# Kernel tuning notes

Hardware: AMD Instinct MI355X
Metric: run time of the kernel (lower is better)

Reference implementation:

```python
import jax, jax.numpy as jnp
import numpy as np

HEADS = 4
DIM_HEAD = 32


def setup_inputs() -> dict:
    key = jax.random.key(0)
    k1, k2, k3, k4 = jax.random.split(key, 4)
    b, dim, t = 8, 64, 16384
    inner = HEADS * DIM_HEAD  # 128
    x = jax.random.normal(k1, (b, dim, t), dtype=jnp.float32)
    # Conv1d(dim, inner*3, kernel=1, bias=False) -> weight (3*inner, dim)
    w_qkv = jax.random.normal(k2, (3 * inner, dim), dtype=jnp.float32) * (1.0 / np.sqrt(dim))
    # Conv1d(inner, dim, kernel=1) -> weight (dim, inner), bias (dim,)
    w_out = jax.random.normal(k3, (dim, inner), dtype=jnp.float32) * (1.0 / np.sqrt(inner))
    b_out = jax.random.normal(k4, (dim,), dtype=jnp.float32) * 0.01
    return {"x": x, "w_qkv": w_qkv, "w_out": w_out, "b_out": b_out}


def reference(x, w_qkv, w_out, b_out):
    b, c, t = x.shape
    h, dh = HEADS, DIM_HEAD
    # 1x1 conv == per-timestep matmul: (b, 3*inner, t)
    qkv = jnp.einsum('oc,bct->bot', w_qkv, x)
    q, k, v = jnp.split(qkv, 3, axis=1)
    q = q.reshape(b, h, dh, t)
    k = k.reshape(b, h, dh, t)
    v = v.reshape(b, h, dh, t)
    q = jax.nn.softmax(q, axis=-1)   # softmax over time
    k = jax.nn.softmax(k, axis=-2)   # softmax over head-dim d
    # einsum('bhdt,bhds->bhds', k, v): sums k over t, broadcast-scales v
    context = jnp.einsum('bhdt,bhds->bhds', k, v)
    # einsum('bhdt,bhds->bhdt', q, context): sums context over s, scales q
    out = jnp.einsum('bhdt,bhds->bhdt', q, context)
    out = out.reshape(b, h * dh, t)
    # to_out 1x1 conv with bias
    return jnp.einsum('oc,bct->bot', w_out, out) + b_out[None, :, None]
```

## Files before the change

kernel.cpp:

```cpp
#include <hip/hip_runtime.h>
#include <math.h>


typedef short short8 __attribute__((ext_vector_type(8)));
typedef short short4s __attribute__((ext_vector_type(4)));
typedef float f32x4 __attribute__((ext_vector_type(4)));

namespace {
constexpr int NB = 8;
constexpr int NC = 64;
constexpr int NT = 16384;
constexpr int NI = 128;
constexpr int TBK = 256;
constexpr int CPB = NT / TBK;
constexpr int NBLK = NB * CPB;
constexpr int XSP = 72;
constexpr int PTP = 136;
constexpr int PT  = 32;
constexpr int REP = 8;

constexpr int WS_ZQ   = 0;
constexpr int WS_KSUM = WS_ZQ + REP * NB * NI;
constexpr int WS_XSUM = WS_KSUM + REP * NB * NI;
constexpr int WS_NFLOAT = WS_XSUM + REP * NB * NC;
}

__device__ __forceinline__ unsigned short f2bf(float f) {
  unsigned u = __float_as_uint(f);
  u += 0x7fffu + ((u >> 16) & 1u);
  return (unsigned short)(u >> 16);
}

template <bool XS>
__device__ __forceinline__ void stage_x(const float* __restrict__ xb, int t0,
                                        unsigned short* xs, float* xsum_dst, int tid) {
  const int c = tid >> 2, tq = tid & 3;
  const float4* xr = (const float4*)(xb + (size_t)c * NT + t0);
  float s = 0.f;
#pragma unroll 4
  for (int i = 0; i < 16; ++i) {
    const int tv = tq + 4 * i;
    float4 v = xr[tv];
    if (XS) s += (v.x + v.y) + (v.z + v.w);
    const int t = 4 * tv;
    xs[(t + 0) * XSP + c] = f2bf(v.x);
    xs[(t + 1) * XSP + c] = f2bf(v.y);
    xs[(t + 2) * XSP + c] = f2bf(v.z);
    xs[(t + 3) * XSP + c] = f2bf(v.w);
  }
  if (XS) {
    s += __shfl_xor(s, 1, 64);
    s += __shfl_xor(s, 2, 64);
    if (tq == 0) atomicAdd(xsum_dst + c, s);
  }
}

__device__ __forceinline__ void load_aq(const float* __restrict__ wqkv, int w,
                                        int lm, int quad, short8 aq[2][2]) {
#pragma unroll
  for (int tile = 0; tile < 2; ++tile)
#pragma unroll
    for (int s = 0; s < 2; ++s) {
      const float* pq = wqkv + (size_t)(32 * w + tile * 16 + lm) * NC + s * 32 + quad * 8;
#pragma unroll
      for (int j = 0; j < 8; ++j) aq[tile][s][j] = (short)f2bf(pq[j]);
    }
}

__global__ __launch_bounds__(256) void la_stats(
    const float* __restrict__ x, const float* __restrict__ wqkv,
    float* __restrict__ ws)
{
  __shared__ __align__(16) unsigned short xs[TBK * XSP];

  const int bid = blockIdx.x;
  const int b = bid >> 6, chunk = bid & 63;
  const int rep = chunk & (REP - 1);
  const int tid = threadIdx.x, lane = tid & 63;
  const int w = __builtin_amdgcn_readfirstlane(tid >> 6);
  const int lm = lane & 15, quad = lane >> 4;
  const float* xb = x + (size_t)b * NC * NT;

  stage_x<true>(xb, chunk * TBK, xs, ws + WS_XSUM + (rep * NB + b) * NC, tid);

  short8 aq[2][2], ak[2][2];
  load_aq(wqkv, w, lm, quad, aq);
#pragma unroll
  for (int tile = 0; tile < 2; ++tile)
#pragma unroll
    for (int s = 0; s < 2; ++s) {
      const float* pk = wqkv + (size_t)(NI + 32 * w + tile * 16 + lm) * NC + s * 32 + quad * 8;
#pragma unroll
      for (int j = 0; j < 8; ++j) ak[tile][s][j] = (short)f2bf(pk[j]);
    }

  float zq_acc[2][4] = {};
  float ks_acc[2][4] = {};
  __syncthreads();

  for (int tc = 0; tc < TBK / 16; ++tc) {
    short8 bf[2];
#pragma unroll
    for (int s = 0; s < 2; ++s)
      bf[s] = *(const short8*)&xs[(tc * 16 + lm) * XSP + s * 32 + quad * 8];
    f32x4 cq[2] = {{0,0,0,0},{0,0,0,0}}, ck[2] = {{0,0,0,0},{0,0,0,0}};
#pragma unroll
    for (int tile = 0; tile < 2; ++tile)
#pragma unroll
      for (int s = 0; s < 2; ++s) {
        cq[tile] = __builtin_amdgcn_mfma_f32_16x16x32_bf16(aq[tile][s], bf[s], cq[tile], 0, 0, 0);
        ck[tile] = __builtin_amdgcn_mfma_f32_16x16x32_bf16(ak[tile][s], bf[s], ck[tile], 0, 0, 0);
      }
    float ke[2][4];
    float zt = 0.f;
#pragma unroll
    for (int tile = 0; tile < 2; ++tile)
#pragma unroll
      for (int r = 0; r < 4; ++r) {
        zq_acc[tile][r] += __expf(cq[tile][r]);
        float e = __expf(ck[tile][r]);
        ke[tile][r] = e;
        zt += e;
      }
    zt += __shfl_xor(zt, 16, 64);
    zt += __shfl_xor(zt, 32, 64);
    const float rz = __builtin_amdgcn_rcpf(zt);
#pragma unroll
    for (int tile = 0; tile < 2; ++tile)
#pragma unroll
      for (int r = 0; r < 4; ++r)
        ks_acc[tile][r] = fmaf(ke[tile][r], rz, ks_acc[tile][r]);
  }

#pragma unroll
  for (int tile = 0; tile < 2; ++tile)
#pragma unroll
    for (int r = 0; r < 4; ++r) {
      float a = zq_acc[tile][r], k = ks_acc[tile][r];
#pragma unroll
      for (int off = 1; off < 16; off <<= 1) {
        a += __shfl_xor(a, off, 64);
        k += __shfl_xor(k, off, 64);
      }
      if (lm == 0) {
        const int c = 32 * w + tile * 16 + quad * 4 + r;
        atomicAdd(ws + WS_ZQ + (rep * NB + b) * NI + c, a);
        atomicAdd(ws + WS_KSUM + (rep * NB + b) * NI + c, k);
      }
    }
}

__global__ __launch_bounds__(256) void la_out(
    const float* __restrict__ x, const float* __restrict__ wqkv,
    const float* __restrict__ wout, const float* __restrict__ bout,
    const float* __restrict__ ws, float* __restrict__ y)
{
  __shared__ __align__(16) unsigned short xs[TBK * XSP];
  __shared__ __align__(16) unsigned short pt[PT * PTP];
  __shared__ float scale_s[NI];
  __shared__ float xsum_s[NC];

  const int bid = blockIdx.x;
  const int b = bid >> 6, chunk = bid & 63;
  const int tid = threadIdx.x, lane = tid & 63;
  const int w = __builtin_amdgcn_readfirstlane(tid >> 6);
  const int lm = lane & 15, quad = lane >> 4;
  const int t0 = chunk * TBK;
  const float* xb = x + (size_t)b * NC * NT;

  stage_x<false>(xb, t0, xs, nullptr, tid);

  if (tid < NC) {
    float s = 0.f;
#pragma unroll
    for (int rp = 0; rp < REP; ++rp) s += ws[WS_XSUM + (rp * NB + b) * NC + tid];
    xsum_s[tid] = s;
  }
  __syncthreads();
  if (tid < NI) {
    float vs = 0.f;
    const float* wv = wqkv + (size_t)(2 * NI + tid) * NC;
#pragma unroll 8
    for (int cc = 0; cc < NC; ++cc) vs = fmaf(wv[cc], xsum_s[cc], vs);
    float zq_t = 0.f, ks_t = 0.f;
#pragma unroll
    for (int rp = 0; rp < REP; ++rp) {
      zq_t += ws[WS_ZQ + (rp * NB + b) * NI + tid];
      ks_t += ws[WS_KSUM + (rp * NB + b) * NI + tid];
    }
    scale_s[tid] = ks_t * vs / zq_t;
  }
  __syncthreads();

  short8 aq[2][2];
  load_aq(wqkv, w, lm, quad, aq);
  short8 aw[4];
  {
    const int o = 16 * w + lm;
#pragma unroll
    for (int s = 0; s < 4; ++s) {
      const float* wo = wout + (size_t)o * NI + s * 32 + quad * 8;
#pragma unroll
      for (int j = 0; j < 8; ++j)
        aw[s][j] = (short)f2bf(wo[j] * scale_s[s * 32 + quad * 8 + j]);
    }
  }
  float bias[4];
#pragma unroll
  for (int r = 0; r < 4; ++r) bias[r] = bout[16 * w + quad * 4 + r];

  for (int sub = 0; sub < TBK / PT; ++sub) {
    for (int tc = 0; tc < PT / 16; ++tc) {
      const int tl = sub * PT + tc * 16;
      short8 bf[2];
#pragma unroll
      for (int s = 0; s < 2; ++s)
        bf[s] = *(const short8*)&xs[(tl + lm) * XSP + s * 32 + quad * 8];
      f32x4 cq[2] = {{0,0,0,0},{0,0,0,0}};
#pragma unroll
      for (int tile = 0; tile < 2; ++tile)
#pragma unroll
        for (int s = 0; s < 2; ++s)
          cq[tile] = __builtin_amdgcn_mfma_f32_16x16x32_bf16(aq[tile][s], bf[s], cq[tile], 0, 0, 0);
#pragma unroll
      for (int tile = 0; tile < 2; ++tile) {
        short4s pv;
#pragma unroll
        for (int r = 0; r < 4; ++r) pv[r] = (short)f2bf(__expf(cq[tile][r]));
        *(short4s*)&pt[(tc * 16 + lm) * PTP + 32 * w + tile * 16 + quad * 4] = pv;
      }
    }
    __syncthreads();
    for (int tc = 0; tc < PT / 16; ++tc) {
      short8 bp[4];
#pragma unroll
      for (int s = 0; s < 4; ++s)
        bp[s] = *(const short8*)&pt[(tc * 16 + lm) * PTP + s * 32 + quad * 8];
      f32x4 acc = {bias[0], bias[1], bias[2], bias[3]};
#pragma unroll
      for (int s = 0; s < 4; ++s)
        acc = __builtin_amdgcn_mfma_f32_16x16x32_bf16(aw[s], bp[s], acc, 0, 0, 0);
#pragma unroll
      for (int r = 0; r < 4; ++r)
        y[((size_t)b * NC + 16 * w + quad * 4 + r) * NT + t0 + sub * PT + tc * 16 + lm] = acc[r];
    }
    __syncthreads();
  }
}

extern "C" void kernel_launch(void* const* d_in, const int* in_sizes, int n_in,
                              void* d_out, int out_size, void* d_ws, size_t ws_size,
                              hipStream_t stream)
{
  const float* x    = (const float*)d_in[0];
  const float* wqkv = (const float*)d_in[1];
  const float* wout = (const float*)d_in[2];
  const float* bout = (const float*)d_in[3];
  float* y  = (float*)d_out;
  float* ws = (float*)d_ws;

  if (ws_size < (size_t)WS_NFLOAT * sizeof(float)) return;

  hipMemsetAsync(ws, 0, (size_t)WS_NFLOAT * sizeof(float), stream);
  la_stats<<<dim3(NBLK), 256, 0, stream>>>(x, wqkv, ws);
  la_out<<<dim3(NBLK), 256, 0, stream>>>(x, wqkv, wout, bout, ws, y);
}
```

Baseline: 114.1 us.

## Halve la_out tile to 128 timesteps and double-buffer exp tile with one barrier

The output kernel now processes 128 timesteps per block instead of 256, so it launches twice as many blocks (1024). The probability tile is ping-pong buffered in shared memory and the next x fragment is prefetched, which cuts the synchronisation to one barrier per 16-step slice instead of two per 32-step sub-tile. The goal is more blocks for latency hiding, a smaller shared-memory footprint for better occupancy, and fewer barriers. In exchange, each extra block repeats the per-block setup work: reducing the stats, computing the scale, and converting the weights.

New measurement: 118.9 us. 4.3% more time.

```diff
diff --git a/kernel.cpp b/kernel.cpp
--- a/kernel.cpp
+++ b/kernel.cpp
@@ -11,12 +11,12 @@
 constexpr int NC = 64;
 constexpr int NT = 16384;
 constexpr int NI = 128;
-constexpr int TBK = 256;
-constexpr int CPB = NT / TBK;
-constexpr int NBLK = NB * CPB;
+constexpr int TBK1 = 256;
+constexpr int NBLK1 = NB * (NT / TBK1);
+constexpr int TBK2 = 128;
+constexpr int NBLK2 = NB * (NT / TBK2);
 constexpr int XSP = 72;
 constexpr int PTP = 136;
-constexpr int PT  = 32;
 constexpr int REP = 8;
 
 constexpr int WS_ZQ   = 0;
@@ -31,14 +31,14 @@
   return (unsigned short)(u >> 16);
 }
 
-template <bool XS>
+template <int NV4, bool XS>
 __device__ __forceinline__ void stage_x(const float* __restrict__ xb, int t0,
                                         unsigned short* xs, float* xsum_dst, int tid) {
   const int c = tid >> 2, tq = tid & 3;
   const float4* xr = (const float4*)(xb + (size_t)c * NT + t0);
   float s = 0.f;
 #pragma unroll 4
-  for (int i = 0; i < 16; ++i) {
+  for (int i = 0; i < NV4; ++i) {
     const int tv = tq + 4 * i;
     float4 v = xr[tv];
     if (XS) s += (v.x + v.y) + (v.z + v.w);
@@ -71,7 +71,7 @@
     const float* __restrict__ x, const float* __restrict__ wqkv,
     float* __restrict__ ws)
 {
-  __shared__ __align__(16) unsigned short xs[TBK * XSP];
+  __shared__ __align__(16) unsigned short xs[TBK1 * XSP];
 
   const int bid = blockIdx.x;
   const int b = bid >> 6, chunk = bid & 63;
@@ -81,7 +81,7 @@
   const int lm = lane & 15, quad = lane >> 4;
   const float* xb = x + (size_t)b * NC * NT;
 
-  stage_x<true>(xb, chunk * TBK, xs, ws + WS_XSUM + (rep * NB + b) * NC, tid);
+  stage_x<16, true>(xb, chunk * TBK1, xs, ws + WS_XSUM + (rep * NB + b) * NC, tid);
 
   short8 aq[2][2], ak[2][2];
   load_aq(wqkv, w, lm, quad, aq);
@@ -98,7 +98,7 @@
   float ks_acc[2][4] = {};
   __syncthreads();
 
-  for (int tc = 0; tc < TBK / 16; ++tc) {
+  for (int tc = 0; tc < TBK1 / 16; ++tc) {
     short8 bf[2];
 #pragma unroll
     for (int s = 0; s < 2; ++s)
@@ -155,20 +155,20 @@
     const float* __restrict__ wout, const float* __restrict__ bout,
     const float* __restrict__ ws, float* __restrict__ y)
 {
-  __shared__ __align__(16) unsigned short xs[TBK * XSP];
-  __shared__ __align__(16) unsigned short pt[PT * PTP];
+  __shared__ __align__(16) unsigned short xs[TBK2 * XSP];
+  __shared__ __align__(16) unsigned short pt[2][16 * PTP];
   __shared__ float scale_s[NI];
   __shared__ float xsum_s[NC];
 
   const int bid = blockIdx.x;
-  const int b = bid >> 6, chunk = bid & 63;
+  const int b = bid >> 7, chunk = bid & 127;
   const int tid = threadIdx.x, lane = tid & 63;
   const int w = __builtin_amdgcn_readfirstlane(tid >> 6);
   const int lm = lane & 15, quad = lane >> 4;
-  const int t0 = chunk * TBK;
+  const int t0 = chunk * TBK2;
   const float* xb = x + (size_t)b * NC * NT;
 
-  stage_x<false>(xb, t0, xs, nullptr, tid);
+  stage_x<8, false>(xb, t0, xs, nullptr, tid);
 
   if (tid < NC) {
     float s = 0.f;
@@ -208,43 +208,45 @@
   float bias[4];
 #pragma unroll
   for (int r = 0; r < 4; ++r) bias[r] = bout[16 * w + quad * 4 + r];
-
-  for (int sub = 0; sub < TBK / PT; ++sub) {
-    for (int tc = 0; tc < PT / 16; ++tc) {
-      const int tl = sub * PT + tc * 16;
-      short8 bf[2];
+  __syncthreads();
+
+  short8 bf[2];
+#pragma unroll
+  for (int s = 0; s < 2; ++s)
+    bf[s] = *(const short8*)&xs[(size_t)lm * XSP + s * 32 + quad * 8];
+
+  for (int tc = 0; tc < TBK2 / 16; ++tc) {
+    f32x4 cq[2] = {{0,0,0,0},{0,0,0,0}};
+#pragma unroll
+    for (int tile = 0; tile < 2; ++tile)
 #pragma unroll
       for (int s = 0; s < 2; ++s)
-        bf[s] = *(const short8*)&xs[(tl + lm) * XSP + s * 32 + quad * 8];
-      f32x4 cq[2] = {{0,0,0,0},{0,0,0,0}};
-#pragma unroll
-      for (int tile = 0; tile < 2; ++tile)
-#pragma unroll
-        for (int s = 0; s < 2; ++s)
-          cq[tile] = __builtin_amdgcn_mfma_f32_16x16x32_bf16(aq[tile][s], bf[s], cq[tile], 0, 0, 0);
-#pragma unroll
-      for (int tile = 0; tile < 2; ++tile) {
-        short4s pv;
-#pragma unroll
-        for (int r = 0; r < 4; ++r) pv[r] = (short)f2bf(__expf(cq[tile][r]));
-        *(short4s*)&pt[(tc * 16 + lm) * PTP + 32 * w + tile * 16 + quad * 4] = pv;
-      }
+        cq[tile] = __builtin_amdgcn_mfma_f32_16x16x32_bf16(aq[tile][s], bf[s], cq[tile], 0, 0, 0);
+    unsigned short* ptc = &pt[tc & 1][0];
+#pragma unroll
+    for (int tile = 0; tile < 2; ++tile) {
+      short4s pv;
+#pragma unroll
+      for (int r = 0; r < 4; ++r) pv[r] = (short)f2bf(__expf(cq[tile][r]));
+      *(short4s*)&ptc[(size_t)lm * PTP + 32 * w + tile * 16 + quad * 4] = pv;
+    }
+    if (tc < TBK2 / 16 - 1) {
+#pragma unroll
+      for (int s = 0; s < 2; ++s)
+        bf[s] = *(const short8*)&xs[((tc + 1) * 16 + lm) * XSP + s * 32 + quad * 8];
     }
     __syncthreads();
-    for (int tc = 0; tc < PT / 16; ++tc) {
-      short8 bp[4];
-#pragma unroll
-      for (int s = 0; s < 4; ++s)
-        bp[s] = *(const short8*)&pt[(tc * 16 + lm) * PTP + s * 32 + quad * 8];
-      f32x4 acc = {bias[0], bias[1], bias[2], bias[3]};
-#pragma unroll
-      for (int s = 0; s < 4; ++s)
-        acc = __builtin_amdgcn_mfma_f32_16x16x32_bf16(aw[s], bp[s], acc, 0, 0, 0);
-#pragma unroll
-      for (int r = 0; r < 4; ++r)
-        y[((size_t)b * NC + 16 * w + quad * 4 + r) * NT + t0 + sub * PT + tc * 16 + lm] = acc[r];
-    }
-    __syncthreads();
+    short8 bp[4];
+#pragma unroll
+    for (int s = 0; s < 4; ++s)
+      bp[s] = *(const short8*)&ptc[(size_t)lm * PTP + s * 32 + quad * 8];
+    f32x4 acc = {bias[0], bias[1], bias[2], bias[3]};
+#pragma unroll
+    for (int s = 0; s < 4; ++s)
+      acc = __builtin_amdgcn_mfma_f32_16x16x32_bf16(aw[s], bp[s], acc, 0, 0, 0);
+#pragma unroll
+    for (int r = 0; r < 4; ++r)
+      y[((size_t)b * NC + 16 * w + quad * 4 + r) * NT + t0 + tc * 16 + lm] = acc[r];
   }
 }
 
@@ -262,6 +264,6 @@
   if (ws_size < (size_t)WS_NFLOAT * sizeof(float)) return;
 
   hipMemsetAsync(ws, 0, (size_t)WS_NFLOAT * sizeof(float), stream);
-  la_stats<<<dim3(NBLK), 256, 0, stream>>>(x, wqkv, ws);
-  la_out<<<dim3(NBLK), 256, 0, stream>>>(x, wqkv, wout, bout, ws, y);
-}
+  la_stats<<<dim3(NBLK1), 256, 0, stream>>>(x, wqkv, ws);
+  la_out<<<dim3(NBLK2), 256, 0, stream>>>(x, wqkv, wout, bout, ws, y);
+}
```
